# Kernel optimization log

Measured on AMD Instinct MI355X. Metric: run time of the kernel, lower is better.

## Reference

```python
import jax, jax.numpy as jnp
import numpy as np

B, T, D, H, S, C = 4, 2048, 1024, 16, 64, 64
LN_EPS = 1e-5
GN_EPS = 1e-5


def _layernorm(x, g, b):
    m = x.mean(-1, keepdims=True)
    v = ((x - m) ** 2).mean(-1, keepdims=True)
    return (x - m) * jax.lax.rsqrt(v + LN_EPS) * g + b


def _act_quant_ste(x):
    # clip_val computed on detached activations (matches x.detach() in torch)
    clip_val = jnp.clip(jnp.abs(jax.lax.stop_gradient(x)).mean(-1, keepdims=True), 1e-8) * 2.5
    scale = clip_val / 127.0
    xs = x / scale
    xc = jnp.clip(xs, -127.0, 127.0)
    xq = jax.lax.stop_gradient(jnp.round(xc) - xs) + xs  # straight-through round
    return xq * scale


def _weight_quant_ste(w):
    scale = jnp.clip(jnp.abs(jax.lax.stop_gradient(w)).mean(), 1e-8)
    wn = w / scale
    wc = jnp.clip(wn, -1.0, 1.0)
    wq = jax.lax.stop_gradient(jnp.round(wc) - wn) + wn  # ternary STE
    return wq * scale


def _bitlinear(x, w, g, b):
    xq = _act_quant_ste(_layernorm(x, g, b))
    wq = _weight_quant_ste(w)
    return xq @ wq.T


def _wkv_train(r, k, v, log_decay, u):
    # r,k,v: (B,H,T,S). Chunked WKV recurrence, chunk size C, state (B,H,S,S).
    dt = r.dtype
    w = jnp.exp(-jnp.exp(log_decay))            # (H,S)
    u_exp = jnp.exp(u)                          # (H,S)
    log_w = jnp.log(jnp.clip(w, 1e-38))
    t = jnp.arange(C, dtype=dt)
    # faithful to torch: diff[a,b] = clamp(t[b]-t[a],0), mask[a,b] = (t[b] >= t[a])
    diff = jnp.clip(t[None, :] - t[:, None], 0.0)
    mask = (t[None, :] >= t[:, None]).astype(dt)
    M = mask[:, :, None, None] * jnp.exp(diff[:, :, None, None] * log_w[None, None])  # (C,C,H,S)
    decay_cross = jnp.transpose(jnp.exp((t + 1.0)[:, None, None] * log_w[None]), (1, 0, 2))  # (H,C,S)
    decay_to_end = jnp.exp((C - 1.0 - t)[:, None, None] * log_w[None])  # (C,H,S)
    w_C = jnp.exp(C * log_w)  # (H,S)

    def chunk(state, rkv):
        r_c, k_c, v_c = rkv                                      # (B,H,C,S)
        kv = k_c[..., :, None] * v_c[..., None, :]               # (B,H,C,S,S)
        A = jnp.einsum('tihs,bhiso->bhtso', M, kv)               # intra-chunk
        A = A + decay_cross[None, :, :, :, None] * state[:, :, None, :, :]  # cross-chunk
        A = A + u_exp[None, :, None, :, None] * kv               # bonus term
        y_c = jnp.einsum('bhts,bhtso->bhto', r_c, A)             # (B,H,C,S)
        new_state = w_C[None, :, :, None] * state + jnp.einsum('chs,bhcso->bhso', decay_to_end, kv)
        return new_state, y_c

    chunk = jax.checkpoint(chunk)  # mirrors torch gradient checkpointing per chunk
    nC = T // C
    resh = lambda a: jnp.transpose(a.reshape(B, H, nC, C, S), (2, 0, 1, 3, 4))
    state0 = jnp.zeros((B, H, S, S), dt)
    _, ys = jax.lax.scan(chunk, state0, (resh(r), resh(k), resh(v)))  # ys: (nC,B,H,C,S)
    return jnp.transpose(ys, (1, 2, 0, 3, 4)).reshape(B, H, T, S)


def reference(x, mu_r, mu_k, mu_v, mu_g, log_decay, u, proj_w, ln_g, ln_b, gn_g, gn_b):
    # token shift: previous token, zero-padded at t=0
    xs = jnp.pad(x, ((0, 0), (1, 0), (0, 0)))[:, :-1]
    xx = xs - x

    def proj(inp, i):
        return _bitlinear(inp, proj_w[i], ln_g[i], ln_b[i])

    to_heads = lambda a: jnp.transpose(a.reshape(B, T, H, S), (0, 2, 1, 3))
    r = to_heads(proj(x + xx * mu_r, 0))
    k = to_heads(proj(x + xx * mu_k, 1))
    v = to_heads(proj(x + xx * mu_v, 2))
    g = proj(x + xx * mu_g, 3)

    y = _wkv_train(r, k, v, log_decay, u)                        # (B,H,T,S)
    y = jnp.transpose(y, (0, 2, 1, 3)).reshape(B, T, D)

    # GroupNorm(H groups over D) applied per (b,t) position
    yg = y.reshape(B, T, H, S)
    m = yg.mean(-1, keepdims=True)
    va = ((yg - m) ** 2).mean(-1, keepdims=True)
    yn = ((yg - m) * jax.lax.rsqrt(va + GN_EPS)).reshape(B, T, D)
    y = yn * gn_g + gn_b

    y = y * jax.nn.silu(g)
    return proj(y, 4)


def setup_inputs() -> dict:
    key = jax.random.key(0)
    ks = jax.random.split(key, 8)
    lid, n_layer = 16, 32
    base_decay = -4.0 + 3.0 * (lid / (n_layer - 1))
    ld = base_decay + 2.0 * (jnp.arange(S, dtype=jnp.float32) / max(S - 1, 1))
    log_decay = jnp.broadcast_to(ld, (H, S)).astype(jnp.float32)
    mu = lambda k: jax.random.uniform(k, (1, 1, D), jnp.float32, -1e-4, 1e-4)
    return {
        'x': jax.random.normal(ks[0], (B, T, D), jnp.float32),
        'mu_r': mu(ks[1]),
        'mu_k': mu(ks[2]),
        'mu_v': mu(ks[3]),
        'mu_g': mu(ks[4]),
        'log_decay': log_decay,
        'u': jax.random.normal(ks[5], (H, S), jnp.float32) * 0.02,
        'proj_w': jax.random.normal(ks[6], (5, D, D), jnp.float32) * 0.02,
        'ln_g': jnp.ones((5, D), jnp.float32),
        'ln_b': jnp.zeros((5, D), jnp.float32),
        'gn_g': jnp.ones((D,), jnp.float32),
        'gn_b': jnp.zeros((D,), jnp.float32),
    }
```

## Files before the change

### kernel.cpp

```cpp
#include <hip/hip_runtime.h>
#include <hip/hip_bf16.h>

#define BB 4
#define TT 2048
#define DD 1024
#define HH 16
#define SS 64
#define CH 64
#define NC (TT/CH)
#define M_ROWS (BB*TT)
#define COL 68

typedef __hip_bfloat16 bf16;
using int4v  = __attribute__((ext_vector_type(4))) int;
using short8 = __attribute__((ext_vector_type(8))) short;
using f32x4  = __attribute__((ext_vector_type(4))) float;

#if defined(__has_builtin)
#if __has_builtin(__builtin_amdgcn_global_load_lds)
#define HAVE_GLL 1
#endif
#if __has_builtin(__builtin_amdgcn_mfma_i32_16x16x64_i8)
#define HAVE_I8K64 1
#endif
#endif

#ifdef HAVE_GLL
static __device__ __forceinline__ void gload16(const void* g, void* l) {
  __builtin_amdgcn_global_load_lds(
      (const __attribute__((address_space(1))) void*)g,
      (__attribute__((address_space(3))) void*)l, 16, 0, 0);
}
#endif

static __device__ __forceinline__ float wave_sum(float v) {
  #pragma unroll
  for (int d = 1; d < 64; d <<= 1) v += __shfl_xor(v, d);
  return v;
}

static __device__ __forceinline__ float block_sum4(float v, float* slot, int tid) {
  float w = wave_sum(v);
  if ((tid & 63) == 0) slot[tid >> 6] = w;
  __syncthreads();
  return slot[0] + slot[1] + slot[2] + slot[3];
}

static __device__ __forceinline__ int pack4(int a, int b, int c, int d) {
  return (a & 0xff) | ((b & 0xff) << 8) | ((c & 0xff) << 16) | ((d & 0xff) << 24);
}

static __device__ __forceinline__ unsigned packsplit(float f) {
  unsigned b  = __float_as_uint(f);
  unsigned hb = b & 0xffff0000u;
  float fl = f - __uint_as_float(hb);
  unsigned lb = __float_as_uint(fl) >> 16;
  return hb | lb;
}

static __device__ __forceinline__ void unpk8(const unsigned* q, short8& h, short8& l) {
  uint4 q0 = *(const uint4*)q;
  uint4 q1 = *(const uint4*)(q + 4);
  unsigned ar[8] = {q0.x, q0.y, q0.z, q0.w, q1.x, q1.y, q1.z, q1.w};
  #pragma unroll
  for (int e = 0; e < 8; e++) {
    h[e] = (short)(ar[e] >> 16);
    l[e] = (short)(ar[e] & 0xffffu);
  }
}

__global__ __launch_bounds__(64) void k_tab(const float* __restrict__ log_decay,
                                            const float* __restrict__ u,
                                            float* __restrict__ P1t,
                                            float* __restrict__ P2t,
                                            float* __restrict__ K1Ft,
                                            float* __restrict__ K2Ft,
                                            float* __restrict__ EUt) {
  int blk = blockIdx.x;
  int h = blk >> 6, t = blk & 63;
  int s = threadIdx.x;
  float d = expf(log_decay[h * SS + s]);
  size_t idx = (size_t)blk * SS + s;
  P1t[idx]  = expf(d * (float)t);
  P2t[idx]  = expf(-d * (float)(t + 1));
  K1Ft[idx] = expf(-d * (float)t);
  K2Ft[idx] = expf(-d * (float)(63 - t));
  if (t == 0) EUt[h * SS + s] = expf(u[h * SS + s]);
}

__global__ __launch_bounds__(256) void k_wscale_part(const float* __restrict__ w,
                                                     double* __restrict__ wpart) {
  __shared__ double red[256];
  int i = blockIdx.x, b = blockIdx.y, tid = threadIdx.x;
  const float* base = w + (size_t)i * DD * DD + (size_t)b * 16384;
  double s = 0.0;
  #pragma unroll
  for (int j = 0; j < 64; j++) s += (double)fabsf(base[tid + j * 256]);
  red[tid] = s; __syncthreads();
  for (int o = 128; o > 0; o >>= 1) {
    if (tid < o) red[tid] += red[tid + o];
    __syncthreads();
  }
  if (tid == 0) wpart[i * 64 + b] = red[0];
}

__global__ __launch_bounds__(64) void k_wscale_fin(const double* __restrict__ wpart,
                                                   float* __restrict__ wscale) {
  int i = blockIdx.x;
  if (threadIdx.x == 0) {
    double s = 0.0;
    for (int b = 0; b < 64; b++) s += wpart[i * 64 + b];
    wscale[i] = fmaxf((float)(s * (1.0 / (DD * DD))), 1e-8f);
  }
}

__global__ __launch_bounds__(256) void k_wquant(const float* __restrict__ w,
                                                const float* __restrict__ wscale,
                                                char* __restrict__ wq) {
  int idx4 = (blockIdx.x * 256 + threadIdx.x) * 4;
  int i = idx4 >> 20;
  float ws = wscale[i];
  float4 w4 = *(const float4*)&w[idx4];
  float vals[4] = {w4.x, w4.y, w4.z, w4.w};
  int q[4];
  #pragma unroll
  for (int j = 0; j < 4; j++) {
    float wn = fminf(fmaxf(vals[j] / ws, -1.f), 1.f);
    q[j] = (int)rintf(wn);
  }
  *(int*)&wq[idx4] = pack4(q[0], q[1], q[2], q[3]);
}

__global__ __launch_bounds__(256) void k_prep_quant(
    const float* __restrict__ x, const float* __restrict__ mu_r,
    const float* __restrict__ mu_k, const float* __restrict__ mu_v,
    const float* __restrict__ mu_g, const float* __restrict__ ln_g,
    const float* __restrict__ ln_b, char* __restrict__ xq,
    float* __restrict__ ascale) {
  __shared__ float slots[12 * 4];
  int m = blockIdx.x, tid = threadIdx.x;
  int t = m & (TT - 1);
  const float* xr = x + (size_t)m * DD;
  int d4 = tid * 4;
  float4 xv4 = *(const float4*)&xr[d4];
  float4 xs4 = (t > 0) ? *(const float4*)&xr[d4 - DD]
                       : (float4){0.f, 0.f, 0.f, 0.f};
  float xv[4] = {xv4.x, xv4.y, xv4.z, xv4.w};
  float xs[4] = {xs4.x, xs4.y, xs4.z, xs4.w};
  const float* mus[4] = {mu_r, mu_k, mu_v, mu_g};
  #pragma unroll 1
  for (int i = 0; i < 4; i++) {
    float4 mu4 = *(const float4*)&mus[i][d4];
    float mu[4] = {mu4.x, mu4.y, mu4.z, mu4.w};
    float inp[4];
    #pragma unroll
    for (int j = 0; j < 4; j++) inp[j] = xv[j] + (xs[j] - xv[j]) * mu[j];
    float mean = block_sum4(inp[0] + inp[1] + inp[2] + inp[3],
                            &slots[(i * 3 + 0) * 4], tid) * (1.f / DD);
    float var = 0.f;
    #pragma unroll
    for (int j = 0; j < 4; j++) { float dv = inp[j] - mean; var += dv * dv; }
    var = block_sum4(var, &slots[(i * 3 + 1) * 4], tid) * (1.f / DD);
    float rstd = 1.f / sqrtf(var + 1e-5f);
    float4 lg4 = *(const float4*)&ln_g[i * DD + d4];
    float4 lb4 = *(const float4*)&ln_b[i * DD + d4];
    float lg[4] = {lg4.x, lg4.y, lg4.z, lg4.w};
    float lb[4] = {lb4.x, lb4.y, lb4.z, lb4.w};
    float ln[4]; float aabs = 0.f;
    #pragma unroll
    for (int j = 0; j < 4; j++) {
      ln[j] = (inp[j] - mean) * rstd * lg[j] + lb[j];
      aabs += fabsf(ln[j]);
    }
    float meanabs = block_sum4(aabs, &slots[(i * 3 + 2) * 4], tid) * (1.f / DD);
    float scale = fmaxf(meanabs, 1e-8f) * 2.5f * (1.f / 127.f);
    int q[4];
    #pragma unroll
    for (int j = 0; j < 4; j++)
      q[j] = (int)rintf(fminf(fmaxf(ln[j] / scale, -127.f), 127.f));
    *(int*)&xq[((size_t)i * M_ROWS + m) * DD + d4] = pack4(q[0], q[1], q[2], q[3]);
    if (tid == 0) ascale[i * M_ROWS + m] = scale;
  }
}

__global__ __launch_bounds__(256) void k_gemm(
    const char* __restrict__ Axq, const char* __restrict__ Wq,
    const float* __restrict__ ascale, const float* __restrict__ wscale,
    int projbase, float* __restrict__ outF) {
  __shared__ __align__(16) char As[2][128 * 64];
  __shared__ __align__(16) char Bs[2][128 * 64];
  int tid = threadIdx.x;
  int wvid = tid >> 6, lane = tid & 63;
  int wm = wvid >> 1, wn = wvid & 1;
  int m0 = blockIdx.x * 128, n0 = blockIdx.y * 128;
  int z = blockIdx.z;
  int proj = projbase + z;
  const char* Ap = Axq + ((size_t)z * M_ROWS + m0) * DD;
  const char* Wp = Wq + ((size_t)proj * DD + n0) * DD;
  int4v acc[4][4];
  #pragma unroll
  for (int i = 0; i < 4; i++)
    #pragma unroll
    for (int j = 0; j < 4; j++) acc[i][j] = (int4v){0, 0, 0, 0};
  int row = tid >> 2, col16 = (tid & 3) * 16;
  int frow = lane & 15, fq16 = (lane >> 4) * 16;

  auto stage = [&](int k0, int buf) {
    #pragma unroll
    for (int q = 0; q < 2; q++) {
#ifdef HAVE_GLL
      gload16(&Ap[(size_t)(q * 64 + row) * DD + k0 + col16],
              &As[buf][q * 4096 + tid * 16]);
      gload16(&Wp[(size_t)(q * 64 + row) * DD + k0 + col16],
              &Bs[buf][q * 4096 + tid * 16]);
#else
      *(uint4*)&As[buf][(q * 64 + row) * 64 + col16] =
          *(const uint4*)&Ap[(size_t)(q * 64 + row) * DD + k0 + col16];
      *(uint4*)&Bs[buf][(q * 64 + row) * 64 + col16] =
          *(const uint4*)&Wp[(size_t)(q * 64 + row) * DD + k0 + col16];
#endif
    }
  };

  stage(0, 0);
  __syncthreads();
  int cur = 0;
  for (int k0 = 0; k0 < DD; k0 += 64) {
    if (k0 + 64 < DD) stage(k0 + 64, cur ^ 1);
#ifdef HAVE_I8K64
    int4v af[4], bfr[4];
    #pragma unroll
    for (int i = 0; i < 4; i++)
      af[i] = *(const int4v*)&As[cur][(64 * wm + 16 * i + frow) * 64 + fq16];
    #pragma unroll
    for (int j = 0; j < 4; j++)
      bfr[j] = *(const int4v*)&Bs[cur][(64 * wn + 16 * j + frow) * 64 + fq16];
    #pragma unroll
    for (int i = 0; i < 4; i++)
      #pragma unroll
      for (int j = 0; j < 4; j++)
        acc[i][j] = __builtin_amdgcn_mfma_i32_16x16x64_i8(af[i], bfr[j], acc[i][j], 0, 0, 0);
#else
    int fq8 = (lane >> 4) * 8;
    long afl[4][2], bfl[4][2];
    #pragma unroll
    for (int i = 0; i < 4; i++)
      #pragma unroll
      for (int h = 0; h < 2; h++)
        afl[i][h] = *(const long*)&As[cur][(64 * wm + 16 * i + frow) * 64 + h * 32 + fq8];
    #pragma unroll
    for (int j = 0; j < 4; j++)
      #pragma unroll
      for (int h = 0; h < 2; h++)
        bfl[j][h] = *(const long*)&Bs[cur][(64 * wn + 16 * j + frow) * 64 + h * 32 + fq8];
    #pragma unroll
    for (int i = 0; i < 4; i++)
      #pragma unroll
      for (int j = 0; j < 4; j++)
        #pragma unroll
        for (int h = 0; h < 2; h++)
          acc[i][j] = __builtin_amdgcn_mfma_i32_16x16x32_i8(afl[i][h], bfl[j][h], acc[i][j], 0, 0, 0);
#endif
    if (k0 + 64 < DD) {
      __syncthreads();
      cur ^= 1;
    }
  }
  const float* asc = ascale + (size_t)z * M_ROWS + m0;
  float wsc = wscale[proj];
  int col = lane & 15, rg = lane >> 4;
  #pragma unroll
  for (int i = 0; i < 4; i++) {
    #pragma unroll
    for (int r = 0; r < 4; r++) {
      int mm = 64 * wm + 16 * i + rg * 4 + r;
      float s = asc[mm] * wsc;
      #pragma unroll
      for (int j = 0; j < 4; j++) {
        int nn = 64 * wn + 16 * j + col;
        outF[((size_t)z * M_ROWS + m0 + mm) * DD + (n0 + nn)] = (float)acc[i][j][r] * s;
      }
    }
  }
}

__global__ __launch_bounds__(256) void k_inj_mm(const float* __restrict__ rkvg,
                                                const float* __restrict__ K2Ft,
                                                float* __restrict__ states) {
#if defined(__HIP_DEVICE_COMPILE__)
  __shared__ __align__(16) unsigned k2t[64 * COL];
  __shared__ __align__(16) unsigned vtsh[64 * COL];
  int blk = blockIdx.x, tid = threadIdx.x;
  int n = blk & (NC - 1), h = (blk >> 5) & (HH - 1), b = blk >> 9;
  size_t rowbase = ((size_t)b * TT + n * CH) * DD + h * SS;
  const float* Kp = rkvg + (size_t)1 * M_ROWS * DD + rowbase;
  const float* Vp = rkvg + (size_t)2 * M_ROWS * DD + rowbase;
  const float* K2h = K2Ft + (size_t)h * SS * SS;

  int s_me = tid & 63, c0 = tid >> 6;
  #pragma unroll 4
  for (int j = 0; j < 16; j++) {
    int c = c0 + 4 * j;
    float kv = Kp[(size_t)c * DD + s_me];
    float vv = Vp[(size_t)c * DD + s_me];
    k2t[s_me * COL + c] = packsplit(kv * K2h[(size_t)c * SS + s_me]);
    vtsh[s_me * COL + c] = packsplit(vv);
  }
  __syncthreads();

  int wid = tid >> 6, lane = tid & 63;
  int s_row = wid * 16 + (lane & 15);
  int koff = (lane >> 4) * 8;
  short8 ah[2], al[2];
  #pragma unroll
  for (int kh = 0; kh < 2; kh++)
    unpk8(&k2t[s_row * COL + kh * 32 + koff], ah[kh], al[kh]);

  float* st = states + (size_t)blk * SS * SS;
  #pragma unroll 1
  for (int ot = 0; ot < 4; ot++) {
    int o_row = ot * 16 + (lane & 15);
    f32x4 acc = {0.f, 0.f, 0.f, 0.f};
    #pragma unroll
    for (int kh = 0; kh < 2; kh++) {
      short8 vh, vl;
      unpk8(&vtsh[o_row * COL + kh * 32 + koff], vh, vl);
      acc = __builtin_amdgcn_mfma_f32_16x16x32_bf16(ah[kh], vh, acc, 0, 0, 0);
      acc = __builtin_amdgcn_mfma_f32_16x16x32_bf16(ah[kh], vl, acc, 0, 0, 0);
      acc = __builtin_amdgcn_mfma_f32_16x16x32_bf16(al[kh], vh, acc, 0, 0, 0);
    }
    #pragma unroll
    for (int rr = 0; rr < 4; rr++) {
      int s = wid * 16 + (lane >> 4) * 4 + rr;
      int o = ot * 16 + (lane & 15);
      st[(size_t)s * SS + o] = acc[rr];
    }
  }
#endif
}

__global__ __launch_bounds__(256) void k_scan(const float* __restrict__ log_decay,
                                              float* __restrict__ states) {
  int blk = blockIdx.x;
  int bh = blk >> 4, sb = blk & 15;
  int h = bh & (HH - 1);
  int tid = threadIdx.x;
  int js = tid >> 6, o = tid & 63;
  int s = sb * 4 + js;
  float wC = expf(-64.f * expf(log_decay[h * SS + s]));
  float* base = states + (size_t)bh * NC * SS * SS + (size_t)s * SS + o;
  float inj[NC];
  #pragma unroll
  for (int n = 0; n < NC; n++) inj[n] = base[(size_t)n * SS * SS];
  float cur = 0.f;
  #pragma unroll
  for (int n = 0; n < NC; n++) {
    base[(size_t)n * SS * SS] = cur;
    cur = fmaf(wC, cur, inj[n]);
  }
}

__global__ __launch_bounds__(256) void k_wkv_mm(const float* __restrict__ rkvg,
                                                const float* __restrict__ states,
                                                const float* __restrict__ P1t,
                                                const float* __restrict__ P2t,
                                                const float* __restrict__ K1Ft,
                                                const float* __restrict__ EUt,
                                                float* __restrict__ Y) {
#if defined(__HIP_DEVICE_COMPILE__)
  __shared__ __align__(16) float    rsh[64 * COL];
  __shared__ __align__(16) unsigned k1sh[64 * COL];
  __shared__ __align__(16) unsigned vtsh[64 * COL];
  unsigned* Pls = (unsigned*)rsh;

  int blk = blockIdx.x, tid = threadIdx.x;
  int n = blk & (NC - 1), h = (blk >> 5) & (HH - 1), b = blk >> 9;
  size_t rowbase = ((size_t)b * TT + n * CH) * DD + h * SS;
  const float* Rp = rkvg + rowbase;
  const float* Kp = rkvg + (size_t)1 * M_ROWS * DD + rowbase;
  const float* Vp = rkvg + (size_t)2 * M_ROWS * DD + rowbase;
  const float* stp = states + (size_t)blk * SS * SS;
  const float* P1h = P1t + (size_t)h * SS * SS;
  const float* P2h = P2t + (size_t)h * SS * SS;
  const float* K1h = K1Ft + (size_t)h * SS * SS;

  int s_me = tid & 63, c0 = tid >> 6;
  float stv[16];
  #pragma unroll 4
  for (int j = 0; j < 16; j++) {
    int c = c0 + 4 * j;
    float rv = Rp[(size_t)c * DD + s_me];
    float kv = Kp[(size_t)c * DD + s_me];
    float vv = Vp[(size_t)c * DD + s_me];
    stv[j] = stp[(size_t)c * SS + s_me];
    rsh[c * COL + s_me] = rv;
    k1sh[c * COL + s_me] = packsplit(kv * K1h[(size_t)c * SS + s_me]);
    vtsh[s_me * COL + c] = packsplit(vv);
  }
  __syncthreads();

  int wid = tid >> 6, lane = tid & 63;
  int t_row = wid * 16 + (lane & 15);
  int koff = (lane >> 4) * 8;

  short8 a1h[2], a1l[2], a2h[2], a2l[2];
  #pragma unroll
  for (int kh = 0; kh < 2; kh++) {
    int sb0 = kh * 32 + koff;
    size_t tb = (size_t)t_row * SS + sb0;
    float4 p1a = *(const float4*)&P1h[tb], p1b = *(const float4*)&P1h[tb + 4];
    float4 p2a = *(const float4*)&P2h[tb], p2b = *(const float4*)&P2h[tb + 4];
    float4 rva = *(const float4*)&rsh[t_row * COL + sb0];
    float4 rvb = *(const float4*)&rsh[t_row * COL + sb0 + 4];
    float p1[8] = {p1a.x, p1a.y, p1a.z, p1a.w, p1b.x, p1b.y, p1b.z, p1b.w};
    float p2[8] = {p2a.x, p2a.y, p2a.z, p2a.w, p2b.x, p2b.y, p2b.z, p2b.w};
    float rv[8] = {rva.x, rva.y, rva.z, rva.w, rvb.x, rvb.y, rvb.z, rvb.w};
    #pragma unroll
    for (int e = 0; e < 8; e++) {
      unsigned u1 = packsplit(rv[e] * p1[e]);
      unsigned u2 = packsplit(rv[e] * p2[e]);
      a1h[kh][e] = (short)(u1 >> 16); a1l[kh][e] = (short)(u1 & 0xffffu);
      a2h[kh][e] = (short)(u2 >> 16); a2l[kh][e] = (short)(u2 & 0xffffu);
    }
  }

  #pragma unroll 1
  for (int it = 0; it < 4; it++) {
    int i_row = it * 16 + (lane & 15);
    f32x4 acc = {0.f, 0.f, 0.f, 0.f};
    f32x4 accu = {0.f, 0.f, 0.f, 0.f};
    bool anyKeep = (it >= wid);
    bool diag = (it == wid);
    if (anyKeep) {
      #pragma unroll
      for (int kh = 0; kh < 2; kh++) {
        const unsigned* q = &k1sh[i_row * COL + kh * 32 + koff];
        uint4 q0 = *(const uint4*)q;
        uint4 q1 = *(const uint4*)(q + 4);
        unsigned ar[8] = {q0.x, q0.y, q0.z, q0.w, q1.x, q1.y, q1.z, q1.w};
        short8 bh, bl;
        #pragma unroll
        for (int e = 0; e < 8; e++) {
          bh[e] = (short)(ar[e] >> 16);
          bl[e] = (short)(ar[e] & 0xffffu);
        }
        acc = __builtin_amdgcn_mfma_f32_16x16x32_bf16(a1h[kh], bh, acc, 0, 0, 0);
        acc = __builtin_amdgcn_mfma_f32_16x16x32_bf16(a1h[kh], bl, acc, 0, 0, 0);
        acc = __builtin_amdgcn_mfma_f32_16x16x32_bf16(a1l[kh], bh, acc, 0, 0, 0);
        if (diag) {
          int sb0 = kh * 32 + koff;
          float4 eua = *(const float4*)&EUt[h * SS + sb0];
          float4 eub = *(const float4*)&EUt[h * SS + sb0 + 4];
          float eu[8] = {eua.x, eua.y, eua.z, eua.w, eub.x, eub.y, eub.z, eub.w};
          short8 bhu, blu;
          #pragma unroll
          for (int e = 0; e < 8; e++) {
            float k1f = __uint_as_float(ar[e] & 0xffff0000u)
                      + __uint_as_float((ar[e] & 0xffffu) << 16);
            unsigned pu = packsplit(k1f * eu[e]);
            bhu[e] = (short)(pu >> 16); blu[e] = (short)(pu & 0xffffu);
          }
          accu = __builtin_amdgcn_mfma_f32_16x16x32_bf16(a1h[kh], bhu, accu, 0, 0, 0);
          accu = __builtin_amdgcn_mfma_f32_16x16x32_bf16(a1h[kh], blu, accu, 0, 0, 0);
          accu = __builtin_amdgcn_mfma_f32_16x16x32_bf16(a1l[kh], bhu, accu, 0, 0, 0);
        }
      }
    }
    #pragma unroll
    for (int rr = 0; rr < 4; rr++) {
      int trow = wid * 16 + (lane >> 4) * 4 + rr;
      int icol = it * 16 + (lane & 15);
      float p = acc[rr];
      p = (icol < trow) ? 0.f : p;
      if (icol == trow) p += accu[rr];
      Pls[trow * COL + icol] = packsplit(p);
    }
  }
  __syncthreads();

  unsigned* stsh = k1sh;
  #pragma unroll
  for (int j = 0; j < 16; j++) {
    int c = c0 + 4 * j;
    stsh[s_me * COL + c] = packsplit(stv[j]);
  }
  __syncthreads();

  float* Yb = Y + ((size_t)b * TT + n * CH) * DD + h * SS;
  #pragma unroll 1
  for (int ot = 0; ot < 4; ot++) {
    int o_row = ot * 16 + (lane & 15);
    f32x4 acc = {0.f, 0.f, 0.f, 0.f};
    #pragma unroll
    for (int kh = 0; kh < 2; kh++) {
      short8 ph, pl, vh, vl, sh2, sl2;
      unpk8(&Pls[t_row * COL + kh * 32 + koff], ph, pl);
      unpk8(&vtsh[o_row * COL + kh * 32 + koff], vh, vl);
      acc = __builtin_amdgcn_mfma_f32_16x16x32_bf16(ph, vh, acc, 0, 0, 0);
      acc = __builtin_amdgcn_mfma_f32_16x16x32_bf16(ph, vl, acc, 0, 0, 0);
      acc = __builtin_amdgcn_mfma_f32_16x16x32_bf16(pl, vh, acc, 0, 0, 0);
      unpk8(&stsh[o_row * COL + kh * 32 + koff], sh2, sl2);
      acc = __builtin_amdgcn_mfma_f32_16x16x32_bf16(a2h[kh], sh2, acc, 0, 0, 0);
      acc = __builtin_amdgcn_mfma_f32_16x16x32_bf16(a2h[kh], sl2, acc, 0, 0, 0);
      acc = __builtin_amdgcn_mfma_f32_16x16x32_bf16(a2l[kh], sh2, acc, 0, 0, 0);
    }
    #pragma unroll
    for (int rr = 0; rr < 4; rr++) {
      int trow = wid * 16 + (lane >> 4) * 4 + rr;
      int oc = ot * 16 + (lane & 15);
      Yb[(size_t)trow * DD + oc] = acc[rr];
    }
  }
#endif
}

__global__ __launch_bounds__(256) void k_post(const float* __restrict__ Y,
                                              const float* __restrict__ G,
                                              const float* __restrict__ gn_g,
                                              const float* __restrict__ gn_b,
                                              const float* __restrict__ lg,
                                              const float* __restrict__ lb,
                                              char* __restrict__ xq4,
                                              float* __restrict__ ascale4) {
  __shared__ float slots[3 * 4];
  __shared__ float gmean[HH], grstd[HH];
  int m = blockIdx.x, tid = threadIdx.x;
  int d4 = tid * 4;
  float4 y4v = *(const float4*)&Y[(size_t)m * DD + d4];
  float4 g4v = *(const float4*)&G[(size_t)m * DD + d4];
  float y4[4] = {y4v.x, y4v.y, y4v.z, y4v.w};
  float g4[4] = {g4v.x, g4v.y, g4v.z, g4v.w};
  {
    float s = y4[0] + y4[1] + y4[2] + y4[3];
    s += __shfl_xor(s, 1); s += __shfl_xor(s, 2);
    s += __shfl_xor(s, 4); s += __shfl_xor(s, 8);
    float mn = s * (1.f / SS);
    float v2 = 0.f;
    #pragma unroll
    for (int q = 0; q < 4; q++) { float dv = y4[q] - mn; v2 += dv * dv; }
    v2 += __shfl_xor(v2, 1); v2 += __shfl_xor(v2, 2);
    v2 += __shfl_xor(v2, 4); v2 += __shfl_xor(v2, 8);
    if ((tid & 15) == 0) {
      gmean[tid >> 4] = mn;
      grstd[tid >> 4] = 1.f / sqrtf(v2 * (1.f / SS) + 1e-5f);
    }
  }
  __syncthreads();
  int hh = tid >> 4;
  float4 gg4 = *(const float4*)&gn_g[d4];
  float4 gb4 = *(const float4*)&gn_b[d4];
  float gg[4] = {gg4.x, gg4.y, gg4.z, gg4.w};
  float gb[4] = {gb4.x, gb4.y, gb4.z, gb4.w};
  float z[4];
  #pragma unroll
  for (int j = 0; j < 4; j++) {
    float yn = (y4[j] - gmean[hh]) * grstd[hh] * gg[j] + gb[j];
    float gv = g4[j];
    z[j] = yn * (gv / (1.f + expf(-gv)));
  }
  float mean = block_sum4(z[0] + z[1] + z[2] + z[3], &slots[0], tid) * (1.f / DD);
  float var = 0.f;
  #pragma unroll
  for (int j = 0; j < 4; j++) { float dv = z[j] - mean; var += dv * dv; }
  var = block_sum4(var, &slots[4], tid) * (1.f / DD);
  float rstd = 1.f / sqrtf(var + 1e-5f);
  float4 lg4 = *(const float4*)&lg[d4];
  float4 lb4 = *(const float4*)&lb[d4];
  float lgv[4] = {lg4.x, lg4.y, lg4.z, lg4.w};
  float lbv[4] = {lb4.x, lb4.y, lb4.z, lb4.w};
  float ln[4]; float aabs = 0.f;
  #pragma unroll
  for (int j = 0; j < 4; j++) {
    ln[j] = (z[j] - mean) * rstd * lgv[j] + lbv[j];
    aabs += fabsf(ln[j]);
  }
  float meanabs = block_sum4(aabs, &slots[8], tid) * (1.f / DD);
  float scale = fmaxf(meanabs, 1e-8f) * 2.5f * (1.f / 127.f);
  int q[4];
  #pragma unroll
  for (int j = 0; j < 4; j++)
    q[j] = (int)rintf(fminf(fmaxf(ln[j] / scale, -127.f), 127.f));
  *(int*)&xq4[(size_t)m * DD + d4] = pack4(q[0], q[1], q[2], q[3]);
  if (tid == 0) ascale4[m] = scale;
}

extern "C" void kernel_launch(void* const* d_in, const int* in_sizes, int n_in,
                              void* d_out, int out_size, void* d_ws, size_t ws_size,
                              hipStream_t stream) {
  const float* x         = (const float*)d_in[0];
  const float* mu_r      = (const float*)d_in[1];
  const float* mu_k      = (const float*)d_in[2];
  const float* mu_v      = (const float*)d_in[3];
  const float* mu_g      = (const float*)d_in[4];
  const float* log_decay = (const float*)d_in[5];
  const float* u         = (const float*)d_in[6];
  const float* proj_w    = (const float*)d_in[7];
  const float* ln_g      = (const float*)d_in[8];
  const float* ln_b      = (const float*)d_in[9];
  const float* gn_g      = (const float*)d_in[10];
  const float* gn_b      = (const float*)d_in[11];
  float* out = (float*)d_out;

  char* p = (char*)d_ws;
  float*  wscale = (float*)p;  p += 256;
  double* wpart  = (double*)p; p += 4096;
  char*   wq     = (char*)p;   p += (size_t)5 * DD * DD;
  float*  ascale = (float*)p;  p += (size_t)5 * M_ROWS * 4;
  char*   U      = p;          p += (size_t)40 * 1024 * 1024;
  char*   xq     = U;
  float*  Y      = (float*)U;
  char*   xq4    = U + (size_t)M_ROWS * DD * 4;
  float*  rkvg   = (float*)p;  p += (size_t)4 * M_ROWS * DD * 4;
  float*  states = (float*)p;  p += (size_t)BB * HH * NC * SS * SS * 4;
  float*  P1t    = (float*)p;  p += (size_t)HH * SS * SS * 4;
  float*  P2t    = (float*)p;  p += (size_t)HH * SS * SS * 4;
  float*  K1Ft   = (float*)p;  p += (size_t)HH * SS * SS * 4;
  float*  K2Ft   = (float*)p;  p += (size_t)HH * SS * SS * 4;
  float*  EUt    = (float*)p;  p += (size_t)HH * SS * 4;

  hipLaunchKernelGGL(k_tab, dim3(HH * SS), dim3(64), 0, stream,
                     log_decay, u, P1t, P2t, K1Ft, K2Ft, EUt);
  hipLaunchKernelGGL(k_wscale_part, dim3(5, 64), dim3(256), 0, stream, proj_w, wpart);
  hipLaunchKernelGGL(k_wscale_fin, dim3(5), dim3(64), 0, stream, wpart, wscale);
  hipLaunchKernelGGL(k_wquant, dim3((5 * DD * DD) / 1024), dim3(256), 0, stream,
                     proj_w, wscale, wq);
  hipLaunchKernelGGL(k_prep_quant, dim3(M_ROWS), dim3(256), 0, stream,
                     x, mu_r, mu_k, mu_v, mu_g, ln_g, ln_b, xq, ascale);
  hipLaunchKernelGGL(k_gemm, dim3(M_ROWS / 128, DD / 128, 4), dim3(256), 0,
                     stream, xq, wq, ascale, wscale, 0, rkvg);
  hipLaunchKernelGGL(k_inj_mm, dim3(BB * HH * NC), dim3(256), 0, stream,
                     rkvg, K2Ft, states);
  hipLaunchKernelGGL(k_scan, dim3(BB * HH * 16), dim3(256), 0, stream,
                     log_decay, states);
  hipLaunchKernelGGL(k_wkv_mm, dim3(BB * HH * NC), dim3(256), 0, stream,
                     rkvg, states, P1t, P2t, K1Ft, EUt, Y);
  hipLaunchKernelGGL(k_post, dim3(M_ROWS), dim3(256), 0, stream,
                     Y, rkvg + (size_t)3 * M_ROWS * DD, gn_g, gn_b,
                     ln_g + 4 * DD, ln_b + 4 * DD,
                     xq4, ascale + 4 * M_ROWS);
  hipLaunchKernelGGL(k_gemm, dim3(M_ROWS / 128, DD / 128, 1), dim3(256), 0,
                     stream, xq4, wq,
                     ascale + 4 * M_ROWS, wscale, 4, out);
}
```

Measured before the change: 332.0 us.

## Enlarge int8 GEMM tiles to 256x256 with triple-buffered swizzled LDS pipeline

The int8 projection GEMM moves from 128x128 tiles with 256 threads and double buffering to 256x256 tiles with 512 threads. It now uses three LDS buffers with an XOR swizzle, and global-to-LDS staging is interleaved with the MFMA passes. It also uses explicit vmcnt waits and s_setprio around the MFMA groups. The aim is more data reuse per tile, fewer LDS bank conflicts and better overlap of loads with compute. The trade-off is a smaller grid: the final single-projection GEMM launches only 128 blocks, which may underfill the GPU.

```diff
diff --git a/kernel.cpp b/kernel.cpp
--- a/kernel.cpp
+++ b/kernel.cpp
@@ -183,97 +183,126 @@
   }
 }
 
-__global__ __launch_bounds__(256) void k_gemm(
+__global__ __launch_bounds__(512) void k_gemm(
     const char* __restrict__ Axq, const char* __restrict__ Wq,
     const float* __restrict__ ascale, const float* __restrict__ wscale,
     int projbase, float* __restrict__ outF) {
-  __shared__ __align__(16) char As[2][128 * 64];
-  __shared__ __align__(16) char Bs[2][128 * 64];
+  __shared__ __align__(16) char As[3][256 * 64];
+  __shared__ __align__(16) char Bs[3][256 * 64];
   int tid = threadIdx.x;
   int wvid = tid >> 6, lane = tid & 63;
-  int wm = wvid >> 1, wn = wvid & 1;
-  int m0 = blockIdx.x * 128, n0 = blockIdx.y * 128;
+  int wm = wvid >> 2, wn = wvid & 3;
+  int m0 = blockIdx.x * 256, n0 = blockIdx.y * 256;
   int z = blockIdx.z;
   int proj = projbase + z;
   const char* Ap = Axq + ((size_t)z * M_ROWS + m0) * DD;
   const char* Wp = Wq + ((size_t)proj * DD + n0) * DD;
-  int4v acc[4][4];
-  #pragma unroll
-  for (int i = 0; i < 4; i++)
+  int4v acc[8][4];
+  #pragma unroll
+  for (int i = 0; i < 8; i++)
     #pragma unroll
     for (int j = 0; j < 4; j++) acc[i][j] = (int4v){0, 0, 0, 0};
-  int row = tid >> 2, col16 = (tid & 3) * 16;
-  int frow = lane & 15, fq16 = (lane >> 4) * 16;
-
-  auto stage = [&](int k0, int buf) {
-    #pragma unroll
-    for (int q = 0; q < 2; q++) {
+
+  int frow = lane & 15, fslot = lane >> 4;
+  int srow_lo = tid >> 2;
+  int sslot0  = tid & 3;
+
+  auto stage_pass = [&](int k0, int q, char* Ad, char* Bd) {
+    int rr = ((q & 1) << 7) + srow_lo;
+    int sl = sslot0 ^ ((rr >> 1) & 3);
+    if (q < 2) {
 #ifdef HAVE_GLL
-      gload16(&Ap[(size_t)(q * 64 + row) * DD + k0 + col16],
-              &As[buf][q * 4096 + tid * 16]);
-      gload16(&Wp[(size_t)(q * 64 + row) * DD + k0 + col16],
-              &Bs[buf][q * 4096 + tid * 16]);
+      gload16(&Ap[(size_t)rr * DD + k0 + sl * 16], &Ad[(q & 1) * 8192 + tid * 16]);
 #else
-      *(uint4*)&As[buf][(q * 64 + row) * 64 + col16] =
-          *(const uint4*)&Ap[(size_t)(q * 64 + row) * DD + k0 + col16];
-      *(uint4*)&Bs[buf][(q * 64 + row) * 64 + col16] =
-          *(const uint4*)&Wp[(size_t)(q * 64 + row) * DD + k0 + col16];
+      *(uint4*)&Ad[(q & 1) * 8192 + tid * 16] =
+          *(const uint4*)&Ap[(size_t)rr * DD + k0 + sl * 16];
+#endif
+    } else {
+#ifdef HAVE_GLL
+      gload16(&Wp[(size_t)rr * DD + k0 + sl * 16], &Bd[(q & 1) * 8192 + tid * 16]);
+#else
+      *(uint4*)&Bd[(q & 1) * 8192 + tid * 16] =
+          *(const uint4*)&Wp[(size_t)rr * DD + k0 + sl * 16];
 #endif
     }
   };
 
-  stage(0, 0);
+  #pragma unroll
+  for (int q = 0; q < 4; q++) stage_pass(0, q, As[0], Bs[0]);
+  #pragma unroll
+  for (int q = 0; q < 4; q++) stage_pass(64, q, As[1], Bs[1]);
+#ifdef HAVE_GLL
+  asm volatile("s_waitcnt vmcnt(4)" ::: "memory");
+  __builtin_amdgcn_s_barrier();
+#else
   __syncthreads();
-  int cur = 0;
-  for (int k0 = 0; k0 < DD; k0 += 64) {
-    if (k0 + 64 < DD) stage(k0 + 64, cur ^ 1);
+#endif
+
+  for (int kt = 0; kt < 16; ++kt) {
+    const char* Abuf = As[kt % 3];
+    const char* Bbuf = Bs[kt % 3];
+    char* Anx = As[(kt + 2) % 3];
+    char* Bnx = Bs[(kt + 2) % 3];
+    int k0n = (kt + 2) * 64;
+    bool do_stage = (kt + 2) < 16;
+    int4v bfr[4];
+    #pragma unroll
+    for (int j = 0; j < 4; j++) {
+      int r = 64 * wn + 16 * j + frow;
+      bfr[j] = *(const int4v*)&Bbuf[r * 64 + (fslot ^ ((r >> 1) & 3)) * 16];
+    }
+    #pragma unroll
+    for (int p = 0; p < 4; p++) {
+      if (do_stage) stage_pass(k0n, p, Anx, Bnx);
+      int4v af[2];
+      #pragma unroll
+      for (int e = 0; e < 2; e++) {
+        int r = 128 * wm + 16 * (2 * p + e) + frow;
+        af[e] = *(const int4v*)&Abuf[r * 64 + (fslot ^ ((r >> 1) & 3)) * 16];
+      }
+      __builtin_amdgcn_s_setprio(1);
 #ifdef HAVE_I8K64
-    int4v af[4], bfr[4];
-    #pragma unroll
-    for (int i = 0; i < 4; i++)
-      af[i] = *(const int4v*)&As[cur][(64 * wm + 16 * i + frow) * 64 + fq16];
-    #pragma unroll
-    for (int j = 0; j < 4; j++)
-      bfr[j] = *(const int4v*)&Bs[cur][(64 * wn + 16 * j + frow) * 64 + fq16];
-    #pragma unroll
-    for (int i = 0; i < 4; i++)
       #pragma unroll
-      for (int j = 0; j < 4; j++)
-        acc[i][j] = __builtin_amdgcn_mfma_i32_16x16x64_i8(af[i], bfr[j], acc[i][j], 0, 0, 0);
+      for (int e = 0; e < 2; e++)
+        #pragma unroll
+        for (int j = 0; j < 4; j++)
+          acc[2 * p + e][j] =
+              __builtin_amdgcn_mfma_i32_16x16x64_i8(af[e], bfr[j], acc[2 * p + e][j], 0, 0, 0);
 #else
-    int fq8 = (lane >> 4) * 8;
-    long afl[4][2], bfl[4][2];
-    #pragma unroll
-    for (int i = 0; i < 4; i++)
       #pragma unroll
-      for (int h = 0; h < 2; h++)
-        afl[i][h] = *(const long*)&As[cur][(64 * wm + 16 * i + frow) * 64 + h * 32 + fq8];
-    #pragma unroll
-    for (int j = 0; j < 4; j++)
-      #pragma unroll
-      for (int h = 0; h < 2; h++)
-        bfl[j][h] = *(const long*)&Bs[cur][(64 * wn + 16 * j + frow) * 64 + h * 32 + fq8];
-    #pragma unroll
-    for (int i = 0; i < 4; i++)
-      #pragma unroll
-      for (int j = 0; j < 4; j++)
+      for (int e = 0; e < 2; e++)
         #pragma unroll
-        for (int h = 0; h < 2; h++)
-          acc[i][j] = __builtin_amdgcn_mfma_i32_16x16x32_i8(afl[i][h], bfl[j][h], acc[i][j], 0, 0, 0);
-#endif
-    if (k0 + 64 < DD) {
+        for (int j = 0; j < 4; j++)
+          #pragma unroll
+          for (int hh2 = 0; hh2 < 2; hh2++) {
+            long a8, b8;
+            memcpy(&a8, ((const char*)&af[e]) + hh2 * 8, 8);
+            memcpy(&b8, ((const char*)&bfr[j]) + hh2 * 8, 8);
+            acc[2 * p + e][j] =
+                __builtin_amdgcn_mfma_i32_16x16x32_i8(a8, b8, acc[2 * p + e][j], 0, 0, 0);
+          }
+#endif
+      __builtin_amdgcn_s_setprio(0);
+    }
+    if (kt < 15) {
+#ifdef HAVE_GLL
+      if (kt + 2 < 16) asm volatile("s_waitcnt vmcnt(4)" ::: "memory");
+      else             asm volatile("s_waitcnt vmcnt(0)" ::: "memory");
+      __builtin_amdgcn_s_barrier();
+#else
       __syncthreads();
-      cur ^= 1;
-    }
-  }
+#endif
+    }
+  }
+
   const float* asc = ascale + (size_t)z * M_ROWS + m0;
   float wsc = wscale[proj];
   int col = lane & 15, rg = lane >> 4;
   #pragma unroll
-  for (int i = 0; i < 4; i++) {
+  for (int i = 0; i < 8; i++) {
     #pragma unroll
     for (int r = 0; r < 4; r++) {
-      int mm = 64 * wm + 16 * i + rg * 4 + r;
+      int mm = 128 * wm + 16 * i + rg * 4 + r;
       float s = asc[mm] * wsc;
       #pragma unroll
       for (int j = 0; j < 4; j++) {
@@ -626,7 +655,7 @@
                      proj_w, wscale, wq);
   hipLaunchKernelGGL(k_prep_quant, dim3(M_ROWS), dim3(256), 0, stream,
                      x, mu_r, mu_k, mu_v, mu_g, ln_g, ln_b, xq, ascale);
-  hipLaunchKernelGGL(k_gemm, dim3(M_ROWS / 128, DD / 128, 4), dim3(256), 0,
+  hipLaunchKernelGGL(k_gemm, dim3(M_ROWS / 256, DD / 256, 4), dim3(512), 0,
                      stream, xq, wq, ascale, wscale, 0, rkvg);
   hipLaunchKernelGGL(k_inj_mm, dim3(BB * HH * NC), dim3(256), 0, stream,
                      rkvg, K2Ft, states);
@@ -638,7 +667,7 @@
                      Y, rkvg + (size_t)3 * M_ROWS * DD, gn_g, gn_b,
                      ln_g + 4 * DD, ln_b + 4 * DD,
                      xq4, ascale + 4 * M_ROWS);
-  hipLaunchKernelGGL(k_gemm, dim3(M_ROWS / 128, DD / 128, 1), dim3(256), 0,
+  hipLaunchKernelGGL(k_gemm, dim3(M_ROWS / 256, DD / 256, 1), dim3(512), 0,
                      stream, xq4, wq,
                      ascale + 4 * M_ROWS, wscale, 4, out);
 }
```

Measured after the change: 333.8 us. About the same (+0.5%).
